# Performance work log

Measured on AMD Instinct MI355X. Metric: run time of the kernel, lower is better.

Reference implementation:

```python
import jax, jax.numpy as jnp
from jax import lax
import numpy as np

DG = 8          # deformable_groups
NF = 64         # num_feat
K = 3
KK = K * K


def conv3(x, w, b):
    # 3x3 'same' conv, NCHW / OIHW
    return lax.conv_general_dilated(x, w, (1, 1), 'SAME',
                                    dimension_numbers=('NCHW', 'OIHW', 'NCHW')) + b[None, :, None, None]


def deform_conv(x, offset, w, b, dg=DG):
    # Offset-only deformable conv (DCN), 3x3, stride 1, pad 1.
    # x: (B,C,H,W); offset: (B, dg*KK*2, H, W) ordered (group, kernel_pos, [dy,dx])
    B, C, H, W = x.shape
    Cg = C // dg
    dt = x.dtype
    off = offset.reshape(B, dg, KK, 2, H, W)
    gy = jnp.arange(H, dtype=dt)[:, None]                      # (H,1)
    gx = jnp.arange(W, dtype=dt)[None, :]                      # (1,W)
    ky = (jnp.arange(KK) // K - 1).astype(dt)[:, None, None]   # (KK,1,1)
    kx = (jnp.arange(KK) % K - 1).astype(dt)[:, None, None]
    py = gy + ky + off[:, :, :, 0]                             # (B,dg,KK,H,W)
    px = gx + kx + off[:, :, :, 1]
    xg = x.reshape(B, dg, Cg, H, W)

    def sample(img, py, px):
        # img (Cg,H,W); py,px (KK,H,W) -> (Cg,KK,H,W); zero padding outside image
        y0 = jnp.floor(py); x0 = jnp.floor(px)
        wy = py - y0; wx = px - x0
        y0 = y0.astype(jnp.int32); x0 = x0.astype(jnp.int32)
        imf = img.reshape(Cg, H * W)

        def gather(yi, xi):
            valid = ((yi >= 0) & (yi < H) & (xi >= 0) & (xi < W)).astype(dt)
            flat = (jnp.clip(yi, 0, H - 1) * W + jnp.clip(xi, 0, W - 1)).reshape(-1)
            return imf[:, flat].reshape(Cg, KK, H, W) * valid

        v00 = gather(y0, x0);     v01 = gather(y0, x0 + 1)
        v10 = gather(y0 + 1, x0); v11 = gather(y0 + 1, x0 + 1)
        return (v00 * (1 - wy) * (1 - wx) + v01 * (1 - wy) * wx
                + v10 * wy * (1 - wx) + v11 * wy * wx)

    samp = jax.vmap(jax.vmap(sample))(xg, py, px)   # (B,dg,Cg,KK,H,W)
    wr = w.reshape(-1, dg, Cg, KK)                  # (Cout,dg,Cg,KK) from (Cout,Cin,3,3)
    out = jnp.einsum('bgckhw,ogck->bohw', samp, wr)
    return out + b[None, :, None, None]


def _forward(pf, xc, cr_w, cr_b, off1_w, off1_b, dc1_w, dc1_b, off2_w, off2_b,
             dc2_w, dc2_b, off3_w, off3_b, dc3_w, dc3_b, off4_w, off4_b,
             dc4_w, dc4_b, rec_w, rec_b):
    B, N, C, H, W = pf.shape
    center = N // 2
    ref = pf[:, center]
    ys = []
    for i in range(N):  # N is a small static frame count (5)
        if i == center:
            ys.append(xc[:, None])
            continue
        supp = pf[:, i]
        fea = conv3(jnp.concatenate([ref, supp], axis=1), cr_w, cr_b)
        fea = deform_conv(fea, conv3(fea, off1_w, off1_b), dc1_w, dc1_b)
        fea = deform_conv(fea, conv3(fea, off2_w, off2_b), dc2_w, dc2_b)
        fea = deform_conv(supp, conv3(fea, off3_w, off3_b), dc3_w, dc3_b)
        aligned = deform_conv(fea, conv3(fea, off4_w, off4_b), dc4_w, dc4_b)
        ys.append(conv3(aligned, rec_w, rec_b)[:, None])
    return jnp.concatenate(ys, axis=1)  # (B, N, 3, H, W)


def setup_inputs() -> dict:
    key = jax.random.key(0)
    ks = jax.random.split(key, 16)
    B, N, C, H, W = 2, 5, NF, 128, 128
    offc = 18 * DG

    def cw(k, cout, cin):
        # matches init_weights: normal(0, sqrt(2 / (k*k*out_channels)))
        return jax.random.normal(k, (cout, cin, 3, 3), jnp.float32) * float(np.sqrt(2.0 / (9 * cout)))

    return {
        'precomputed_features': jax.random.normal(ks[0], (B, N, C, H, W), jnp.float32),
        'x_center': jax.random.normal(ks[1], (B, 3, H, W), jnp.float32),
        'cr_w': cw(ks[2], C, 2 * C), 'cr_b': jnp.zeros((C,), jnp.float32),
        'off1_w': cw(ks[3], offc, C), 'off1_b': jnp.zeros((offc,), jnp.float32),
        'dc1_w': cw(ks[4], C, C), 'dc1_b': jnp.zeros((C,), jnp.float32),
        'off2_w': cw(ks[5], offc, C), 'off2_b': jnp.zeros((offc,), jnp.float32),
        'dc2_w': cw(ks[6], C, C), 'dc2_b': jnp.zeros((C,), jnp.float32),
        'off3_w': cw(ks[7], offc, C), 'off3_b': jnp.zeros((offc,), jnp.float32),
        'dc3_w': cw(ks[8], C, C), 'dc3_b': jnp.zeros((C,), jnp.float32),
        'off4_w': cw(ks[9], offc, C), 'off4_b': jnp.zeros((offc,), jnp.float32),
        'dc4_w': cw(ks[10], C, C), 'dc4_b': jnp.zeros((C,), jnp.float32),
        'rec_w': cw(ks[11], 3, C), 'rec_b': jnp.zeros((3,), jnp.float32),
    }


def reference(precomputed_features, x_center, cr_w, cr_b, off1_w, off1_b, dc1_w, dc1_b,
              off2_w, off2_b, dc2_w, dc2_b, off3_w, off3_b, dc3_w, dc3_b,
              off4_w, off4_b, dc4_w, dc4_b, rec_w, rec_b):
    return _forward(precomputed_features, x_center, cr_w, cr_b, off1_w, off1_b, dc1_w, dc1_b,
                    off2_w, off2_b, dc2_w, dc2_b, off3_w, off3_b, dc3_w, dc3_b,
                    off4_w, off4_b, dc4_w, dc4_b, rec_w, rec_b)
```

## Files before the change

### kernel.cpp

```cpp
#include <hip/hip_runtime.h>

#define HH 128
#define WW 128
#define HWP (HH*WW)
#define NC 64
#define NB 2
#define NN 5
#define OFFC 144
#define NKC 18

typedef __attribute__((ext_vector_type(8))) _Float16 half8;
typedef __attribute__((ext_vector_type(4))) float floatx4;
typedef __attribute__((ext_vector_type(2))) float floatx2;

__global__ __launch_bounds__(256) void copy_center_k(const float* __restrict__ xc,
                                                     float* __restrict__ out) {
    int idx = blockIdx.x * 256 + threadIdx.x;
    const int total = NB * 3 * HWP;
    if (idx >= total) return;
    int b = idx / (3 * HWP);
    int r = idx - b * 3 * HWP;
    out[(size_t)((b * NN + 2) * 3) * HWP + r] = xc[idx];
}

__global__ __launch_bounds__(256) void repack_k(const float* __restrict__ pf,
                                                float* __restrict__ dst, int job0, int is_ref)
{
    __shared__ float T[64][65];
    const int jl = blockIdx.y;
    const float* src;
    if (is_ref) {
        src = pf + (size_t)((jl * NN + 2) * NC) * HWP;
    } else {
        int jg = job0 + jl;
        int b = jg & 1, fi = jg >> 1;
        int frame = fi + (fi >= 2 ? 1 : 0);
        src = pf + (size_t)((b * NN + frame) * NC) * HWP;
    }
    float* d = dst + (size_t)jl * NC * HWP;
    const int p0 = blockIdx.x * 64;
    const int tid = threadIdx.x;
    const int lx = tid & 63, cg4 = tid >> 6;
#pragma unroll
    for (int cc = 0; cc < 16; ++cc) {
        int c = cc * 4 + cg4;
        T[c][lx] = src[(size_t)c * HWP + p0 + lx];
    }
    __syncthreads();
    const int px = tid >> 2, c0 = (tid & 3) * 16;
#pragma unroll
    for (int j = 0; j < 4; ++j) {
        floatx4 v = { T[c0 + j*4 + 0][px], T[c0 + j*4 + 1][px],
                      T[c0 + j*4 + 2][px], T[c0 + j*4 + 3][px] };
        *(floatx4*)(d + (size_t)(p0 + px) * 64 + c0 + j*4) = v;
    }
}

__global__ __launch_bounds__(256) void prew_k(const float* __restrict__ w,
                                              _Float16* __restrict__ wp,
                                              int nct, int nkc, int mode,
                                              int ci_off, int cin_src)
{
    int idx = blockIdx.x * 256 + threadIdx.x;
    if (idx >= nct * nkc * 64) return;
    int lane = idx & 63;
    int kc = (idx >> 6) % nkc;
    int ct = (idx >> 6) / nkc;
    int m = lane & 15, quad = lane >> 4;
    int co = ct * 16 + m;
    union { half8 v; _Float16 e[8]; } ph, pl;
#pragma unroll
    for (int j = 0; j < 8; ++j) {
        int k = kc * 32 + quad * 8 + j;
        float f = 0.f;
        if (mode == 0) {
            int kk = k >> 6, ci = k & 63;
            f = w[((size_t)co * cin_src + ci_off + ci) * 9 + kk];
        } else {
            int r = k / 160, kr = k - r * 160;
            if (kr < 144) {
                int g = r * 2 + kr / 72;
                int rr = kr % 72;
                int kk = rr >> 3, cg = rr & 7;
                f = w[((size_t)co * cin_src + g * 8 + cg) * 9 + kk];
            }
        }
        _Float16 h = (_Float16)f;
        ph.e[j] = h; pl.e[j] = (_Float16)(f - (float)h);
    }
    size_t base = (size_t)((ct * nkc + kc) * 2) * 512;
    *(half8*)(wp + base + lane * 8) = ph.v;
    *(half8*)(wp + base + 512 + lane * 8) = pl.v;
}

template<int NCT, int SRCMODE, int ADD>
__global__ __launch_bounds__(256, 3) void mconv_k(
    const float* __restrict__ src, const float* __restrict__ R,
    const float* __restrict__ S, const _Float16* __restrict__ wp,
    const float* __restrict__ bias, float* __restrict__ out, int job0)
{
    constexpr int PL = 1456;
    constexpr int Ct = NCT * 16;
    const int jl = blockIdx.y, jg = job0 + jl;
    const int b = jg & 1;
    const int tile = blockIdx.x;
    const int ty0 = (tile >> 3) << 3, tx0 = (tile & 7) << 4;
    const int tid = threadIdx.x;
    const int lane = tid & 63;
    const int wq = __builtin_amdgcn_readfirstlane(tid >> 6);
    const int n = lane & 15, quad = lane >> 4;

    const float* s0;
    if (SRCMODE == 0)      s0 = src + (size_t)jl * NC * HWP;
    else if (SRCMODE == 1) s0 = R + (size_t)b * NC * HWP;
    else                   s0 = S + (size_t)jl * NC * HWP;

    __shared__ _Float16 hh[8 * PL];
    __shared__ _Float16 ll[8 * PL];

    for (int t = tid; t < 360; t += 256) {
        int px = t >> 1, hf = t & 1;
        int hy = px / 18, hx = px - hy * 18;
        int gy = ty0 - 1 + hy, gx = tx0 - 1 + hx;
        bool ok = (gy >= 0 && gy < HH && gx >= 0 && gx < WW);
        const float* sp = s0 + (ok ? ((size_t)(gy * WW + gx) * 64) : 0) + hf * 32;
        int lb = px * 8;
#pragma unroll
        for (int c = 0; c < 4; ++c) {
            int cb = hf * 4 + c;
            floatx4 f0 = {0.f,0.f,0.f,0.f}, f1 = {0.f,0.f,0.f,0.f};
            if (ok) {
                f0 = *(const floatx4*)(sp + c * 8);
                f1 = *(const floatx4*)(sp + c * 8 + 4);
            }
            union { half8 v; _Float16 e[8]; } ph, pl;
#pragma unroll
            for (int j = 0; j < 4; ++j) {
                _Float16 h0 = (_Float16)f0[j], h1 = (_Float16)f1[j];
                ph.e[j] = h0;     ph.e[j+4] = h1;
                pl.e[j] = (_Float16)(f0[j] - (float)h0);
                pl.e[j+4] = (_Float16)(f1[j] - (float)h1);
            }
            *(half8*)&hh[cb * PL + lb] = ph.v;
            *(half8*)&ll[cb * PL + lb] = pl.v;
        }
    }
    __syncthreads();

    floatx4 acc0[NCT], acc1[NCT];
#pragma unroll
    for (int ct = 0; ct < NCT; ++ct) {
        acc0[ct] = floatx4{0.f, 0.f, 0.f, 0.f};
        acc1[ct] = floatx4{0.f, 0.f, 0.f, 0.f};
    }
    const int y0 = wq * 2, y1 = y0 + 1;
#pragma unroll
    for (int kc = 0; kc < NKC; ++kc) {
        const int kk = kc >> 1;
        const int dy = kk / 3, dx = kk % 3;
        const int cb = ((kc & 1) << 2) + quad;
        const int ix0 = cb * PL + ((y0 + dy) * 18 + n + dx) * 8;
        const int ix1 = cb * PL + ((y1 + dy) * 18 + n + dx) * 8;
        half8 B0h = *(const half8*)&hh[ix0];
        half8 B0l = *(const half8*)&ll[ix0];
        half8 B1h = *(const half8*)&hh[ix1];
        half8 B1l = *(const half8*)&ll[ix1];
        const _Float16* wk = wp + (size_t)kc * 1024 + lane * 8;
#pragma unroll
        for (int ct = 0; ct < NCT; ++ct) {
            const _Float16* wc = wk + (size_t)ct * NKC * 1024;
            half8 Ah = *(const half8*)wc;
            half8 Al = *(const half8*)(wc + 512);
            acc0[ct] = __builtin_amdgcn_mfma_f32_16x16x32_f16(Ah, B0h, acc0[ct], 0, 0, 0);
            acc0[ct] = __builtin_amdgcn_mfma_f32_16x16x32_f16(Ah, B0l, acc0[ct], 0, 0, 0);
            acc0[ct] = __builtin_amdgcn_mfma_f32_16x16x32_f16(Al, B0h, acc0[ct], 0, 0, 0);
            acc1[ct] = __builtin_amdgcn_mfma_f32_16x16x32_f16(Ah, B1h, acc1[ct], 0, 0, 0);
            acc1[ct] = __builtin_amdgcn_mfma_f32_16x16x32_f16(Ah, B1l, acc1[ct], 0, 0, 0);
            acc1[ct] = __builtin_amdgcn_mfma_f32_16x16x32_f16(Al, B1h, acc1[ct], 0, 0, 0);
        }
    }

    const int oy0 = ty0 + y0, oy1 = ty0 + y1, ox = tx0 + n;
#pragma unroll
    for (int ct = 0; ct < NCT; ++ct) {
        const floatx4 b4 = *(const floatx4*)(bias + ct * 16 + quad * 4);
        float* op0 = out + ((size_t)jl * HWP + (size_t)oy0 * WW + ox) * Ct
                         + ct * 16 + quad * 4;
        float* op1 = out + ((size_t)jl * HWP + (size_t)oy1 * WW + ox) * Ct
                         + ct * 16 + quad * 4;
        floatx4 v0 = acc0[ct], v1 = acc1[ct];
        if (ADD) {
            v0 += *(const floatx4*)op0;
            v1 += *(const floatx4*)op1;
        } else {
            v0 += b4;
            v1 += b4;
        }
        *(floatx4*)op0 = v0;
        *(floatx4*)op1 = v1;
    }
}

__global__ __launch_bounds__(512, 4) void mdeform_k(
    const float* __restrict__ in, const float* __restrict__ off,
    const _Float16* __restrict__ wp, const float* __restrict__ bias,
    float* __restrict__ out, int supp_mode, const float* __restrict__ S)
{
    constexpr int SROW = 166;
    const int jl = blockIdx.y;
    const int tile = blockIdx.x;
    const int ty0 = (tile >> 4) << 3, tx0 = (tile & 15) << 3;
    const int tid = threadIdx.x;
    const int lane = tid & 63;
    const int w8 = __builtin_amdgcn_readfirstlane(tid >> 6);
    const int q4 = w8 >> 1;
    const int sb2 = (w8 & 1) << 1;
    const int n = lane & 15, quad = lane >> 4;

    const float* ibase = supp_mode ? (S + (size_t)jl * NC * HWP)
                                   : (in + (size_t)jl * NC * HWP);
    const float* obase = off + (size_t)jl * OFFC * HWP;

    __shared__ _Float16 sh[64 * SROW];
    __shared__ _Float16 sl[64 * SROW];
    __shared__ float stg[256 * 16];

    for (int e = tid; e < 64 * 16; e += 512) {
        int row = e >> 4, col = 144 + (e & 15);
        sh[row * SROW + col] = (_Float16)0.f;
        sl[row * SROW + col] = (_Float16)0.f;
    }

    floatx4 acc[2];
#pragma unroll
    for (int s = 0; s < 2; ++s) acc[s] = floatx4{0.f, 0.f, 0.f, 0.f};

    for (int r = 0; r < 4; ++r) {
#pragma unroll
        for (int j = 0; j < 2; ++j) {
            int t = tid + (j << 9);
            int slot = t >> 2;
            int qq = t & 3;
            int ry = slot >> 4, rx = slot & 15;
            int gy = ty0 - 4 + ry, gx = tx0 - 4 + rx;
            if ((unsigned)gy < (unsigned)HH && (unsigned)gx < (unsigned)WW) {
                floatx4 v = *(const floatx4*)(ibase + (size_t)(gy * WW + gx) * 64
                                              + r * 16 + qq * 4);
                *(floatx4*)&stg[(slot << 4) + ((qq ^ ((slot >> 1) & 3)) << 2)] = v;
            }
        }
        __syncthreads();
        for (int i = 0; i < 5; ++i) {
            int idx = tid + (i << 9);
            if (idx >= 2304) break;
            int hf = idx & 1;
            int pair = idx >> 1;
            int gl = pair / 576;
            int rem = pair - gl * 576;
            int kk = rem >> 6;
            int px = rem & 63;
            int g = r * 2 + gl;
            int yy = ty0 + (px >> 3), xx = tx0 + (px & 7);
            floatx2 o2 = *(const floatx2*)(obase + (size_t)(yy * WW + xx) * OFFC
                                           + (g * 9 + kk) * 2);
            float pyf = (float)(yy + (kk / 3) - 1) + o2[0];
            float pxf = (float)(xx + (kk % 3) - 1) + o2[1];
            float fy = floorf(pyf), fx = floorf(pxf);
            float wy = pyf - fy, wx = pxf - fx;
            int y0 = (int)fy, x0 = (int)fx;
            int y1 = y0 + 1, x1 = x0 + 1;
            float m00 = (y0 >= 0 && y0 < HH && x0 >= 0 && x0 < WW) ? 1.f : 0.f;
            float m01 = (y0 >= 0 && y0 < HH && x1 >= 0 && x1 < WW) ? 1.f : 0.f;
            float m10 = (y1 >= 0 && y1 < HH && x0 >= 0 && x0 < WW) ? 1.f : 0.f;
            float m11 = (y1 >= 0 && y1 < HH && x1 >= 0 && x1 < WW) ? 1.f : 0.f;
            float w00 = (1.f - wy) * (1.f - wx) * m00;
            float w01 = (1.f - wy) * wx * m01;
            float w10 = wy * (1.f - wx) * m10;
            float w11 = wy * wx * m11;
            int cy0 = min(max(y0, 0), HH - 1), cy1 = min(max(y1, 0), HH - 1);
            int cx0 = min(max(x0, 0), WW - 1), cx1 = min(max(x1, 0), WW - 1);
            const int qc = (gl << 1) + hf;
            int ry0 = cy0 - ty0 + 4, ry1 = cy1 - ty0 + 4;
            int rx0 = cx0 - tx0 + 4, rx1 = cx1 - tx0 + 4;
            bool allin = ((unsigned)ry0 < 16u) & ((unsigned)ry1 < 16u) &
                         ((unsigned)rx0 < 16u) & ((unsigned)rx1 < 16u);
            floatx4 a, b, c, d;
            if (allin) {
                int s00 = (ry0 << 4) + rx0, s01 = (ry0 << 4) + rx1;
                int s10 = (ry1 << 4) + rx0, s11 = (ry1 << 4) + rx1;
                a = *(const floatx4*)&stg[(s00 << 4) + ((qc ^ ((s00 >> 1) & 3)) << 2)];
                b = *(const floatx4*)&stg[(s01 << 4) + ((qc ^ ((s01 >> 1) & 3)) << 2)];
                c = *(const floatx4*)&stg[(s10 << 4) + ((qc ^ ((s10 >> 1) & 3)) << 2)];
                d = *(const floatx4*)&stg[(s11 << 4) + ((qc ^ ((s11 >> 1) & 3)) << 2)];
            } else {
                const int co = g * 8 + hf * 4;
                a = *(const floatx4*)(ibase + (size_t)(cy0 * WW + cx0) * 64 + co);
                b = *(const floatx4*)(ibase + (size_t)(cy0 * WW + cx1) * 64 + co);
                c = *(const floatx4*)(ibase + (size_t)(cy1 * WW + cx0) * 64 + co);
                d = *(const floatx4*)(ibase + (size_t)(cy1 * WW + cx1) * 64 + co);
            }
            floatx4 sv = a * w00 + b * w01 + c * w10 + d * w11;
            union { unsigned u[2]; _Float16 e[4]; } P, L;
#pragma unroll
            for (int j = 0; j < 4; ++j) {
                _Float16 h = (_Float16)sv[j];
                P.e[j] = h;
                L.e[j] = (_Float16)(sv[j] - (float)h);
            }
            int sb = px * SROW + gl * 72 + kk * 8 + hf * 4;
            unsigned* shp = (unsigned*)&sh[sb];
            unsigned* slp = (unsigned*)&sl[sb];
            shp[0] = P.u[0]; shp[1] = P.u[1];
            slp[0] = L.u[0]; slp[1] = L.u[1];
        }
        __syncthreads();
#pragma unroll
        for (int kc5 = 0; kc5 < 5; ++kc5) {
            int kcg = r * 5 + kc5;
            size_t base = (size_t)((q4 * 20 + kcg) * 2) * 512;
            half8 Ah = *(const half8*)(wp + base + lane * 8);
            half8 Al = *(const half8*)(wp + base + 512 + lane * 8);
#pragma unroll
            for (int s = 0; s < 2; ++s) {
                int px = (sb2 + s) * 16 + n;
                const int ix = px * SROW + kc5 * 32 + quad * 8;
                half8 Bh = *(const half8*)&sh[ix];
                half8 Bl = *(const half8*)&sl[ix];
                acc[s] = __builtin_amdgcn_mfma_f32_16x16x32_f16(Ah, Bh, acc[s], 0, 0, 0);
                acc[s] = __builtin_amdgcn_mfma_f32_16x16x32_f16(Ah, Bl, acc[s], 0, 0, 0);
                acc[s] = __builtin_amdgcn_mfma_f32_16x16x32_f16(Al, Bh, acc[s], 0, 0, 0);
            }
        }
    }
    const floatx4 b4 = *(const floatx4*)(bias + q4 * 16 + quad * 4);
#pragma unroll
    for (int s = 0; s < 2; ++s) {
        int px = (sb2 + s) * 16 + n;
        int oy = ty0 + (px >> 3), ox = tx0 + (px & 7);
        float* op = out + ((size_t)jl * HWP + (size_t)oy * WW + ox) * 64
                        + q4 * 16 + quad * 4;
        *(floatx4*)op = acc[s] + b4;
    }
}

__global__ __launch_bounds__(256) void conv3x3_rec_k(
    const float* __restrict__ in, const float* __restrict__ w,
    const float* __restrict__ bias, float* __restrict__ out, int job0)
{
    constexpr int CB = 8;
    constexpr int PITCH = 48;
    constexpr int CH = 18 * PITCH;
    const int jl = blockIdx.y, jg = job0 + jl;
    const int b = jg & 1, fi = jg >> 1;
    const int frame = fi + (fi >= 2 ? 1 : 0);
    const int tile = blockIdx.x;
    const int ty0 = (tile >> 3) << 4, tx0 = (tile & 7) << 4;
    const int tid = threadIdx.x;
    const int tx = tid & 15, ty = tid >> 4;
    const float* srcA = in + (size_t)jl * NC * HWP;

    __shared__ float lds[CB * CH];
    float acc[3] = {bias[0], bias[1], bias[2]};

    for (int cb = 0; cb < NC; cb += CB) {
        __syncthreads();
        for (int e = tid; e < CB * 324; e += 256) {
            int c = e & 7;
            int r = e >> 3;
            int iy = r / 18, ix = r - iy * 18;
            int gy = ty0 - 1 + iy, gx = tx0 - 1 + ix;
            float v = 0.f;
            if (gy >= 0 && gy < HH && gx >= 0 && gx < WW)
                v = srcA[(size_t)(gy * WW + gx) * 64 + cb + c];
            lds[c * CH + iy * PITCH + ix] = v;
        }
        __syncthreads();
#pragma unroll
        for (int c = 0; c < CB; ++c) {
            float t[9];
#pragma unroll
            for (int dy = 0; dy < 3; ++dy)
#pragma unroll
                for (int dx = 0; dx < 3; ++dx)
                    t[dy * 3 + dx] = lds[c * CH + (ty + dy) * PITCH + (tx + dx)];
            int ci = cb + c;
#pragma unroll
            for (int o = 0; o < 3; ++o) {
                const float* wo = w + ((size_t)o * NC + ci) * 9;
#pragma unroll
                for (int kk = 0; kk < 9; ++kk)
                    acc[o] = fmaf(wo[kk], t[kk], acc[o]);
            }
        }
    }
    const int oy = ty0 + ty, ox = tx0 + tx;
#pragma unroll
    for (int o = 0; o < 3; ++o)
        out[((size_t)(b * NN + frame) * 3 + o) * HWP + oy * WW + ox] = acc[o];
}

extern "C" void kernel_launch(void* const* d_in, const int* in_sizes, int n_in,
                              void* d_out, int out_size, void* d_ws, size_t ws_size,
                              hipStream_t stream)
{
    const float* pf    = (const float*)d_in[0];
    const float* xc    = (const float*)d_in[1];
    const float* cr_w  = (const float*)d_in[2];
    const float* cr_b  = (const float*)d_in[3];
    const float* ow[4] = {(const float*)d_in[4],  (const float*)d_in[8],
                          (const float*)d_in[12], (const float*)d_in[16]};
    const float* ob[4] = {(const float*)d_in[5],  (const float*)d_in[9],
                          (const float*)d_in[13], (const float*)d_in[17]};
    const float* dw[4] = {(const float*)d_in[6],  (const float*)d_in[10],
                          (const float*)d_in[14], (const float*)d_in[18]};
    const float* db[4] = {(const float*)d_in[7],  (const float*)d_in[11],
                          (const float*)d_in[15], (const float*)d_in[19]};
    const float* rec_w = (const float*)d_in[20];
    const float* rec_b = (const float*)d_in[21];
    float* out = (float*)d_out;

    const size_t WPC = (size_t)4 * NKC * 1024;
    const size_t WPO = (size_t)9 * NKC * 1024;
    const size_t WPD = (size_t)4 * 20 * 1024;
    _Float16* wp_cr0 = (_Float16*)d_ws;
    _Float16* wp_cr1 = wp_cr0 + WPC;
    _Float16* wp_of[4];
    _Float16* wp_dc[4];
    _Float16* curh = wp_cr1 + WPC;
    for (int i = 0; i < 4; ++i) { wp_of[i] = curh; curh += WPO; }
    for (int i = 0; i < 4; ++i) { wp_dc[i] = curh; curh += WPD; }
    size_t wp_bytes = (size_t)((char*)curh - (char*)d_ws);

    const size_t fplane = (size_t)NC * HWP;
    const size_t oplane = (size_t)OFFC * HWP;
    int JC = 8;
    while (JC > 1 &&
           wp_bytes + (2 + 3 * (size_t)JC) * fplane * 4 + (size_t)JC * oplane * 4 > ws_size)
        JC >>= 1;
    float* R  = (float*)curh;
    float* S  = R  + 2 * fplane;
    float* A  = S  + (size_t)JC * fplane;
    float* Bb = A  + (size_t)JC * fplane;
    float* O  = Bb + (size_t)JC * fplane;

    {
        int nc4 = 4 * NKC * 64, nc9 = 9 * NKC * 64, ncd = 4 * 20 * 64;
        dim3 b4((nc4 + 255) / 256), b9((nc9 + 255) / 256), bd((ncd + 255) / 256);
        prew_k<<<b4, 256, 0, stream>>>(cr_w, wp_cr0, 4, NKC, 0, 0, 128);
        prew_k<<<b4, 256, 0, stream>>>(cr_w, wp_cr1, 4, NKC, 0, 64, 128);
        for (int i = 0; i < 4; ++i) {
            prew_k<<<b9, 256, 0, stream>>>(ow[i], wp_of[i], 9, NKC, 0, 0, 64);
            prew_k<<<bd, 256, 0, stream>>>(dw[i], wp_dc[i], 4, 20, 1, 0, 64);
        }
        repack_k<<<dim3(256, 2), 256, 0, stream>>>(pf, R, 0, 1);
    }

    copy_center_k<<<dim3((NB * 3 * HWP + 255) / 256), 256, 0, stream>>>(xc, out);

    for (int job0 = 0; job0 < 8; job0 += JC) {
        dim3 blk(256);
        dim3 blk512(512);
        dim3 gconv(128, JC), gdef(256, JC), grec(64, JC);
        repack_k<<<dim3(256, JC), blk, 0, stream>>>(pf, S, job0, 0);
        mconv_k<4, 1, 0><<<gconv, blk, 0, stream>>>(nullptr, R, S, wp_cr0, cr_b, A, job0);
        mconv_k<4, 2, 1><<<gconv, blk, 0, stream>>>(nullptr, R, S, wp_cr1, cr_b, A, job0);
        mconv_k<9, 0, 0><<<gconv, blk, 0, stream>>>(A, R, S, wp_of[0], ob[0], O, job0);
        mdeform_k<<<gdef, blk512, 0, stream>>>(A, O, wp_dc[0], db[0], Bb, 0, S);
        mconv_k<9, 0, 0><<<gconv, blk, 0, stream>>>(Bb, R, S, wp_of[1], ob[1], O, job0);
        mdeform_k<<<gdef, blk512, 0, stream>>>(Bb, O, wp_dc[1], db[1], A, 0, S);
        mconv_k<9, 0, 0><<<gconv, blk, 0, stream>>>(A, R, S, wp_of[2], ob[2], O, job0);
        mdeform_k<<<gdef, blk512, 0, stream>>>(nullptr, O, wp_dc[2], db[2], Bb, 1, S);
        mconv_k<9, 0, 0><<<gconv, blk, 0, stream>>>(Bb, R, S, wp_of[3], ob[3], O, job0);
        mdeform_k<<<gdef, blk512, 0, stream>>>(Bb, O, wp_dc[3], db[3], A, 0, S);
        conv3x3_rec_k<<<grec, blk, 0, stream>>>(A, rec_w, rec_b, out, job0);
    }
}
```

Before: 1.220 ms.

## Split mconv output-channel tiles across waves instead of splitting rows

In the 3x3 MFMA conv kernel, each wave now computes all 8 tile rows for its own slice of output-channel tiles, rather than 2 rows for every channel tile. Each wave loads only its share of the split-half weight fragments from global memory once per kernel chunk, which cuts redundant weight traffic by about four times. In exchange, each wave reads all 8 rows of input fragments from LDS, so LDS reads go up about four times, and accumulator register use grows. When the tile count does not divide evenly by four the work is unbalanced: a single-tile output leaves three waves idle, and nine tiles split as 2/2/2/3.

```diff
diff --git a/kernel.cpp b/kernel.cpp
--- a/kernel.cpp
+++ b/kernel.cpp
@@ -101,6 +101,7 @@
 {
     constexpr int PL = 1456;
     constexpr int Ct = NCT * 16;
+    constexpr int MC = (NCT + 3) / 4;
     const int jl = blockIdx.y, jg = job0 + jl;
     const int b = jg & 1;
     const int tile = blockIdx.x;
@@ -109,6 +110,8 @@
     const int lane = tid & 63;
     const int wq = __builtin_amdgcn_readfirstlane(tid >> 6);
     const int n = lane & 15, quad = lane >> 4;
+    const int ct0 = (wq * NCT) >> 2;
+    const int ct1 = ((wq + 1) * NCT) >> 2;
 
     const float* s0;
     if (SRCMODE == 0)      s0 = src + (size_t)jl * NC * HWP;
@@ -147,57 +150,63 @@
     }
     __syncthreads();
 
-    floatx4 acc0[NCT], acc1[NCT];
-#pragma unroll
-    for (int ct = 0; ct < NCT; ++ct) {
-        acc0[ct] = floatx4{0.f, 0.f, 0.f, 0.f};
-        acc1[ct] = floatx4{0.f, 0.f, 0.f, 0.f};
-    }
-    const int y0 = wq * 2, y1 = y0 + 1;
+    floatx4 acc[8][MC];
+#pragma unroll
+    for (int y = 0; y < 8; ++y)
+#pragma unroll
+        for (int cc = 0; cc < MC; ++cc)
+            acc[y][cc] = floatx4{0.f, 0.f, 0.f, 0.f};
+
 #pragma unroll
     for (int kc = 0; kc < NKC; ++kc) {
         const int kk = kc >> 1;
         const int dy = kk / 3, dx = kk % 3;
         const int cb = ((kc & 1) << 2) + quad;
-        const int ix0 = cb * PL + ((y0 + dy) * 18 + n + dx) * 8;
-        const int ix1 = cb * PL + ((y1 + dy) * 18 + n + dx) * 8;
-        half8 B0h = *(const half8*)&hh[ix0];
-        half8 B0l = *(const half8*)&ll[ix0];
-        half8 B1h = *(const half8*)&hh[ix1];
-        half8 B1l = *(const half8*)&ll[ix1];
         const _Float16* wk = wp + (size_t)kc * 1024 + lane * 8;
-#pragma unroll
-        for (int ct = 0; ct < NCT; ++ct) {
-            const _Float16* wc = wk + (size_t)ct * NKC * 1024;
-            half8 Ah = *(const half8*)wc;
-            half8 Al = *(const half8*)(wc + 512);
-            acc0[ct] = __builtin_amdgcn_mfma_f32_16x16x32_f16(Ah, B0h, acc0[ct], 0, 0, 0);
-            acc0[ct] = __builtin_amdgcn_mfma_f32_16x16x32_f16(Ah, B0l, acc0[ct], 0, 0, 0);
-            acc0[ct] = __builtin_amdgcn_mfma_f32_16x16x32_f16(Al, B0h, acc0[ct], 0, 0, 0);
-            acc1[ct] = __builtin_amdgcn_mfma_f32_16x16x32_f16(Ah, B1h, acc1[ct], 0, 0, 0);
-            acc1[ct] = __builtin_amdgcn_mfma_f32_16x16x32_f16(Ah, B1l, acc1[ct], 0, 0, 0);
-            acc1[ct] = __builtin_amdgcn_mfma_f32_16x16x32_f16(Al, B1h, acc1[ct], 0, 0, 0);
-        }
-    }
-
-    const int oy0 = ty0 + y0, oy1 = ty0 + y1, ox = tx0 + n;
-#pragma unroll
-    for (int ct = 0; ct < NCT; ++ct) {
-        const floatx4 b4 = *(const floatx4*)(bias + ct * 16 + quad * 4);
-        float* op0 = out + ((size_t)jl * HWP + (size_t)oy0 * WW + ox) * Ct
-                         + ct * 16 + quad * 4;
-        float* op1 = out + ((size_t)jl * HWP + (size_t)oy1 * WW + ox) * Ct
-                         + ct * 16 + quad * 4;
-        floatx4 v0 = acc0[ct], v1 = acc1[ct];
-        if (ADD) {
-            v0 += *(const floatx4*)op0;
-            v1 += *(const floatx4*)op1;
-        } else {
-            v0 += b4;
-            v1 += b4;
-        }
-        *(floatx4*)op0 = v0;
-        *(floatx4*)op1 = v1;
+        half8 Ah[MC], Al[MC];
+#pragma unroll
+        for (int cc = 0; cc < MC; ++cc) {
+            if (ct0 + cc < ct1) {
+                const _Float16* wc = wk + (size_t)(ct0 + cc) * NKC * 1024;
+                Ah[cc] = *(const half8*)wc;
+                Al[cc] = *(const half8*)(wc + 512);
+            }
+        }
+#pragma unroll
+        for (int y = 0; y < 8; ++y) {
+            const int ix = cb * PL + ((y + dy) * 18 + n + dx) * 8;
+            half8 Bh = *(const half8*)&hh[ix];
+            half8 Bl = *(const half8*)&ll[ix];
+#pragma unroll
+            for (int cc = 0; cc < MC; ++cc) {
+                if (ct0 + cc < ct1) {
+                    acc[y][cc] = __builtin_amdgcn_mfma_f32_16x16x32_f16(Ah[cc], Bh, acc[y][cc], 0, 0, 0);
+                    acc[y][cc] = __builtin_amdgcn_mfma_f32_16x16x32_f16(Ah[cc], Bl, acc[y][cc], 0, 0, 0);
+                    acc[y][cc] = __builtin_amdgcn_mfma_f32_16x16x32_f16(Al[cc], Bh, acc[y][cc], 0, 0, 0);
+                }
+            }
+        }
+    }
+
+    const int ox = tx0 + n;
+#pragma unroll
+    for (int cc = 0; cc < MC; ++cc) {
+        if (ct0 + cc < ct1) {
+            const int ct = ct0 + cc;
+            const floatx4 b4 = *(const floatx4*)(bias + ct * 16 + quad * 4);
+#pragma unroll
+            for (int y = 0; y < 8; ++y) {
+                float* op = out + ((size_t)jl * HWP + (size_t)(ty0 + y) * WW + ox) * Ct
+                                + ct * 16 + quad * 4;
+                floatx4 v = acc[y][cc];
+                if (ADD) {
+                    v += *(const floatx4*)op;
+                } else {
+                    v += b4;
+                }
+                *(floatx4*)op = v;
+            }
+        }
     }
 }
 
```

Measured after the change: 1.433 ms. 17.4% more time.
